# Kernel optimization log

Hardware: AMD Instinct MI355X
Metric: run time of the kernel (lower is better)

Reference implementation:

```python
import jax, jax.numpy as jnp
import numpy as np
import math

N_HEAD = 16
N_KV_HEAD = 4
N_EMBD = 2048
HEAD_DIM = N_EMBD // N_HEAD  # 128
SCALE = 1.0 / math.sqrt(HEAD_DIM)
B, T = 2, 2048


def setup_inputs() -> dict:
    key = jax.random.key(0)
    ks = jax.random.split(key, 5)
    s = 0.02
    x = jax.random.normal(ks[0], (B, T, N_EMBD), dtype=jnp.float32)
    wq = jax.random.normal(ks[1], (N_EMBD, N_EMBD), dtype=jnp.float32) * s
    wk = jax.random.normal(ks[2], (N_KV_HEAD * HEAD_DIM, N_EMBD), dtype=jnp.float32) * s
    wv = jax.random.normal(ks[3], (N_KV_HEAD * HEAD_DIM, N_EMBD), dtype=jnp.float32) * s
    wo = jax.random.normal(ks[4], (N_EMBD, N_EMBD), dtype=jnp.float32) * s
    return {"x": x, "wq": wq, "wk": wk, "wv": wv, "wo": wo}


def _forward(x, wq, wk, wv, wo):
    b, t, _ = x.shape
    # Linear layers: y = x @ W.T  (torch Linear weight is (out,in))
    q = (x @ wq.T).reshape(b, t, N_HEAD, HEAD_DIM).transpose(0, 2, 1, 3)      # (B,H,T,D)
    k = (x @ wk.T).reshape(b, t, N_KV_HEAD, HEAD_DIM).transpose(0, 2, 1, 3)  # (B,Hkv,T,D)
    v = (x @ wv.T).reshape(b, t, N_KV_HEAD, HEAD_DIM).transpose(0, 2, 1, 3)
    groups = N_HEAD // N_KV_HEAD
    k = jnp.repeat(k, groups, axis=1)  # repeat_interleave over head dim -> (B,H,T,D)
    v = jnp.repeat(v, groups, axis=1)
    # Causal mask: True above diagonal (masked-out positions)
    mask = jnp.triu(jnp.ones((t, t), dtype=bool), k=1)[None, None]  # (1,1,T,T)
    scores = jnp.einsum('bhqd,bhkd->bhqk', q, k) * SCALE
    scores = jnp.where(mask, -jnp.inf, scores)
    attn = jax.nn.softmax(scores, axis=-1)
    attn = jnp.where(mask, 0.0, attn)
    y = jnp.einsum('bhqk,bhkd->bhqd', attn, v)       # (B,H,T,D)
    y = y.transpose(0, 2, 1, 3).reshape(b, t, N_EMBD)
    return y @ wo.T


def reference(x, wq, wk, wv, wo):
    return _forward(x, wq, wk, wv, wo)
```

## Files before the change

### kernel.cpp

```cpp
#include <hip/hip_runtime.h>
#include <cstdint>
#include <cstddef>

typedef __bf16 bf16_t;
typedef __bf16 bf16x8 __attribute__((ext_vector_type(8)));
typedef __bf16 bf16x4 __attribute__((ext_vector_type(4)));
typedef float f32x4 __attribute__((ext_vector_type(4)));

#define GL2LDS16(gptr, lptr)                                                   \
  __builtin_amdgcn_global_load_lds(                                            \
      (__attribute__((address_space(1))) void*)(gptr),                         \
      (__attribute__((address_space(3))) void*)(lptr), 16, 0, 0)

__device__ __forceinline__ float fast_exp2(float x) {
  float r;
  asm volatile("v_exp_f32 %0, %1" : "=v"(r) : "v"(x));
  return r;
}

#define BATCH 2
#define T_SEQ 2048
#define NH 16
#define NKV 4
#define HD 128
#define EMB 2048
#define KVDIM (NKV * HD)
#define MROWS (BATCH * T_SEQ)

__global__ void cvt_all(const float4* __restrict__ x,  const float4* __restrict__ wq,
                        const float4* __restrict__ wk, const float4* __restrict__ wv,
                        const float4* __restrict__ wo,
                        bf16x4* __restrict__ xb,  bf16x4* __restrict__ wqb,
                        bf16x4* __restrict__ wkb, bf16x4* __restrict__ wvb,
                        bf16x4* __restrict__ wob) {
  const int blk = blockIdx.x;
  const float4* src;
  bf16x4* dst;
  int base;
  if (blk < 8192)       { src = x;  dst = xb;  base = blk; }
  else if (blk < 12288) { src = wq; dst = wqb; base = blk - 8192; }
  else if (blk < 13312) { src = wk; dst = wkb; base = blk - 12288; }
  else if (blk < 14336) { src = wv; dst = wvb; base = blk - 13312; }
  else                  { src = wo; dst = wob; base = blk - 14336; }
  const int i = base * 256 + threadIdx.x;
  const float4 v = src[i];
  dst[i] = bf16x4{(__bf16)v.x, (__bf16)v.y, (__bf16)v.z, (__bf16)v.w};
}

#define BK8 64
#define NT8 (EMB / BK8)

__global__ __launch_bounds__(512, 2)
void gemm_qkv8(const bf16_t* __restrict__ A,
               const bf16_t* __restrict__ Wq, const bf16_t* __restrict__ Wk,
               const bf16_t* __restrict__ Wv,
               bf16_t* __restrict__ Qb, bf16_t* __restrict__ Kb,
               bf16_t* __restrict__ Vt, float qalpha)
{
  __shared__ bf16_t lds[2][512 * 64];

  const int tid  = threadIdx.x;
  const int lane = tid & 63;
  const int wv   = tid >> 6;
  const int l15  = lane & 15;
  const int lq   = lane >> 4;

  const int bid0 = blockIdx.x;
  const int bid  = (bid0 & 7) * 24 + (bid0 >> 3);
  const int mt = bid / 12, nt = bid % 12;
  const int m0 = mt * 256;

  const bf16_t* Bmat; int ncol0, seg;
  if (nt < 8)       { Bmat = Wq; ncol0 = nt * 256;        seg = 0; }
  else if (nt < 10) { Bmat = Wk; ncol0 = (nt - 8) * 256;  seg = 1; }
  else              { Bmat = Wv; ncol0 = (nt - 10) * 256; seg = 2; }

  const int wm = (wv >> 2) * 128;
  const int wn = (wv & 3) * 64;

  f32x4 acc[8][4] = {};

  auto stage = [&](int dbuf, int tsrc, int h) {
    const int k0 = tsrc * BK8;
    const bf16_t* src = (h < 2) ? A : Bmat;
    const int rbase = (h < 2) ? (m0 + h * 128) : (ncol0 + (h - 2) * 128);
    bf16_t* dst = &lds[dbuf][h * 8192];
#pragma unroll
    for (int r = 0; r < 2; ++r) {
      const int c = r * 512 + tid;
      const int row = c >> 3, p = c & 7;
      const int sb = p ^ (row & 7);
      GL2LDS16(src + (size_t)(rbase + row) * EMB + k0 + sb * 8, dst + c * 8);
    }
  };

  stage(0, 0, 0); stage(0, 0, 1); stage(0, 0, 2); stage(0, 0, 3);
  stage(1, 1, 2); stage(1, 1, 0); stage(1, 1, 3);
  asm volatile("s_waitcnt vmcnt(6)" ::: "memory");
  __builtin_amdgcn_s_barrier();

  bf16x8 a[4][2], b[4][2];

#pragma unroll 1
  for (int tt = 0; tt < NT8; tt += 2) {
#pragma unroll
    for (int u = 0; u < 2; ++u) {
      const int t   = tt + u;
      const int cur = u;
      const int nxt = u ^ 1;
      const int tn1 = (t + 1 < NT8) ? t + 1 : NT8 - 1;
      const int tn2 = (t + 2 < NT8) ? t + 2 : NT8 - 1;

#pragma unroll
      for (int i = 0; i < 4; ++i) {
        const int row = wm + i * 16 + l15;
#pragma unroll
        for (int ks = 0; ks < 2; ++ks)
          a[i][ks] = *(const bf16x8*)&lds[cur][row * 64 + (((ks * 4 + lq) ^ (row & 7)) * 8)];
      }
#pragma unroll
      for (int j = 0; j < 2; ++j) {
        const int row = 256 + wn + j * 16 + l15;
#pragma unroll
        for (int ks = 0; ks < 2; ++ks)
          b[j][ks] = *(const bf16x8*)&lds[cur][row * 64 + (((ks * 4 + lq) ^ (row & 7)) * 8)];
      }
      stage(nxt, tn1, 1);
      __builtin_amdgcn_s_barrier();
      __builtin_amdgcn_s_setprio(1);
#pragma unroll
      for (int ks = 0; ks < 2; ++ks)
#pragma unroll
        for (int i = 0; i < 4; ++i)
#pragma unroll
          for (int j = 0; j < 2; ++j)
            acc[i][j] = __builtin_amdgcn_mfma_f32_16x16x32_bf16(a[i][ks], b[j][ks], acc[i][j], 0, 0, 0);
      __builtin_amdgcn_s_setprio(0);
      __builtin_amdgcn_s_barrier();

#pragma unroll
      for (int j = 2; j < 4; ++j) {
        const int row = 256 + wn + j * 16 + l15;
#pragma unroll
        for (int ks = 0; ks < 2; ++ks)
          b[j][ks] = *(const bf16x8*)&lds[cur][row * 64 + (((ks * 4 + lq) ^ (row & 7)) * 8)];
      }
      __builtin_amdgcn_s_barrier();
      __builtin_amdgcn_s_setprio(1);
#pragma unroll
      for (int ks = 0; ks < 2; ++ks)
#pragma unroll
        for (int i = 0; i < 4; ++i)
#pragma unroll
          for (int j = 2; j < 4; ++j)
            acc[i][j] = __builtin_amdgcn_mfma_f32_16x16x32_bf16(a[i][ks], b[j][ks], acc[i][j], 0, 0, 0);
      __builtin_amdgcn_s_setprio(0);
      __builtin_amdgcn_s_barrier();

#pragma unroll
      for (int i = 0; i < 4; ++i) {
        const int row = wm + (4 + i) * 16 + l15;
#pragma unroll
        for (int ks = 0; ks < 2; ++ks)
          a[i][ks] = *(const bf16x8*)&lds[cur][row * 64 + (((ks * 4 + lq) ^ (row & 7)) * 8)];
      }
      stage(cur, tn2, 2);
      __builtin_amdgcn_s_barrier();
      __builtin_amdgcn_s_setprio(1);
#pragma unroll
      for (int ks = 0; ks < 2; ++ks)
#pragma unroll
        for (int i = 0; i < 4; ++i)
#pragma unroll
          for (int j = 2; j < 4; ++j)
            acc[4 + i][j] = __builtin_amdgcn_mfma_f32_16x16x32_bf16(a[i][ks], b[j][ks], acc[4 + i][j], 0, 0, 0);
      __builtin_amdgcn_s_setprio(0);
      __builtin_amdgcn_s_barrier();

      stage(cur, tn2, 0);
      stage(cur, tn2, 3);
      __builtin_amdgcn_s_barrier();
      __builtin_amdgcn_s_setprio(1);
#pragma unroll
      for (int ks = 0; ks < 2; ++ks)
#pragma unroll
        for (int i = 0; i < 4; ++i)
#pragma unroll
          for (int j = 0; j < 2; ++j)
            acc[4 + i][j] = __builtin_amdgcn_mfma_f32_16x16x32_bf16(a[i][ks], b[j][ks], acc[4 + i][j], 0, 0, 0);
      __builtin_amdgcn_s_setprio(0);
      asm volatile("s_waitcnt vmcnt(6)" ::: "memory");
      __builtin_amdgcn_s_barrier();
    }
  }
  asm volatile("s_waitcnt vmcnt(0)" ::: "memory");

  if (seg == 0) {
#pragma unroll
    for (int i = 0; i < 8; ++i) {
      const int rbase = m0 + wm + i * 16 + lq * 4;
#pragma unroll
      for (int j = 0; j < 4; ++j) {
        const int col = ncol0 + wn + j * 16 + l15;
#pragma unroll
        for (int r = 0; r < 4; ++r)
          Qb[(size_t)(rbase + r) * EMB + col] = (bf16_t)(acc[i][j][r] * qalpha);
      }
    }
  } else if (seg == 1) {
#pragma unroll
    for (int i = 0; i < 8; ++i) {
      const int rbase = m0 + wm + i * 16 + lq * 4;
#pragma unroll
      for (int j = 0; j < 4; ++j) {
        const int col = ncol0 + wn + j * 16 + l15;
#pragma unroll
        for (int r = 0; r < 4; ++r)
          Kb[(size_t)(rbase + r) * KVDIM + col] = (bf16_t)acc[i][j][r];
      }
    }
  } else {
    const int bb = m0 >> 11;
    const int mloc0 = (m0 & 2047) + wm + lq * 4;
#pragma unroll
    for (int i = 0; i < 8; ++i) {
      const int mloc = mloc0 + i * 16;
#pragma unroll
      for (int j = 0; j < 4; ++j) {
        const int d = ncol0 + wn + j * 16 + l15;
        *(bf16x4*)(Vt + (size_t)(bb * KVDIM + d) * T_SEQ + mloc) =
            bf16x4{(__bf16)acc[i][j][0], (__bf16)acc[i][j][1],
                   (__bf16)acc[i][j][2], (__bf16)acc[i][j][3]};
      }
    }
  }
}

__global__ __launch_bounds__(256, 2)
void gemm_out(const bf16_t* __restrict__ A, const bf16_t* __restrict__ Bm,
              float* __restrict__ C, int M, int N, int K)
{
  __shared__ bf16_t As[128 * 64];
  __shared__ bf16_t Bs[128 * 64];

  const int tid  = threadIdx.x;
  const int lane = tid & 63;
  const int wv   = tid >> 6;
  const int m0 = blockIdx.y * 128;
  const int n0 = blockIdx.x * 128;
  const int wm = (wv >> 1) * 64;
  const int wn = (wv & 1) * 64;
  const int l15 = lane & 15;
  const int lq  = lane >> 4;

  f32x4 acc[4][4] = {};
  const int srow = tid >> 3;
  const int scol = (tid & 7) * 8;

  for (int k0 = 0; k0 < K; k0 += 64) {
#pragma unroll
    for (int r = 0; r < 4; ++r) {
      const int row = r * 32 + srow;
      GL2LDS16(A + (size_t)(m0 + row) * K + k0 + scol, As + row * 64 + scol);
    }
#pragma unroll
    for (int r = 0; r < 4; ++r) {
      const int row = r * 32 + srow;
      GL2LDS16(Bm + (size_t)(n0 + row) * K + k0 + scol, Bs + row * 64 + scol);
    }
    __syncthreads();

#pragma unroll
    for (int ks = 0; ks < 2; ++ks) {
      const int kc = ks * 32 + lq * 8;
      bf16x8 af[4], bf[4];
#pragma unroll
      for (int i = 0; i < 4; ++i)
        af[i] = *(const bf16x8*)(As + (wm + i * 16 + l15) * 64 + kc);
#pragma unroll
      for (int j = 0; j < 4; ++j)
        bf[j] = *(const bf16x8*)(Bs + (wn + j * 16 + l15) * 64 + kc);
#pragma unroll
      for (int i = 0; i < 4; ++i)
#pragma unroll
        for (int j = 0; j < 4; ++j)
          acc[i][j] = __builtin_amdgcn_mfma_f32_16x16x32_bf16(af[i], bf[j], acc[i][j], 0, 0, 0);
    }
    __syncthreads();
  }

#pragma unroll
  for (int i = 0; i < 4; ++i) {
    const int rbase = m0 + wm + i * 16 + lq * 4;
#pragma unroll
    for (int j = 0; j < 4; ++j) {
      const int col = n0 + wn + j * 16 + l15;
#pragma unroll
      for (int r = 0; r < 4; ++r)
        C[(size_t)(rbase + r) * N + col] = acc[i][j][r];
    }
  }
}

#define PSTR 72

__global__ __launch_bounds__(256, 2)
void attn_fwd(const bf16_t* __restrict__ Q, const bf16_t* __restrict__ Kg,
              const bf16_t* __restrict__ Vt, bf16_t* __restrict__ Y)
{
  __shared__ bf16_t Ks[2][64 * 128];
  __shared__ bf16_t Vs[2][128 * 64];
  __shared__ bf16_t Ps[4][16 * PSTR];

  const int tid  = threadIdx.x;
  const int lane = tid & 63;
  const int wv   = tid >> 6;
  const int l15  = lane & 15;
  const int lq   = lane >> 4;
  const int h  = blockIdx.y;
  const int b  = blockIdx.z;
  const int hkv = h >> 2;
  bf16_t* Psw = Ps[wv];

  auto stage = [&](int kt, int bufsel) {
    const int base_t = b * T_SEQ + kt * 64;
#pragma unroll
    for (int r = 0; r < 4; ++r) {
      const int c = r * 256 + tid;
      const int row = c >> 4, p = c & 15;
      const int sb = p ^ (row & 7);
      GL2LDS16(Kg + (size_t)(base_t + row) * KVDIM + hkv * HD + sb * 8,
               &Ks[bufsel][c * 8]);
    }
#pragma unroll
    for (int r = 0; r < 4; ++r) {
      const int c = r * 256 + tid;
      const int row = c >> 3, p = c & 7;
      const int sb = p ^ (row & 7);
      GL2LDS16(Vt + (size_t)(b * KVDIM + hkv * HD + row) * T_SEQ + kt * 64 + sb * 8,
               &Vs[bufsel][c * 8]);
    }
  };

#pragma unroll 1
  for (int ph = 0; ph < 2; ++ph) {
    const int qt = ph ? blockIdx.x : (31 - blockIdx.x);
    const int q0 = qt * 64;
    const int nkt = qt + 1;
    const int qabs = q0 + wv * 16 + l15;

    bf16x8 qf[4];
    {
      const bf16_t* qp = Q + ((size_t)(b * T_SEQ + qabs) * NH + h) * HD + lq * 8;
#pragma unroll
      for (int ds = 0; ds < 4; ++ds)
        qf[ds] = *(const bf16x8*)(qp + ds * 32);
    }

    float l_part = 0.f;
    f32x4 o[8];
#pragma unroll
    for (int nb = 0; nb < 8; ++nb) o[nb] = f32x4{0.f, 0.f, 0.f, 0.f};

    __syncthreads();
    stage(0, 0);

    for (int kt = 0; kt < nkt; ++kt) {
      const int cur = kt & 1;
      __syncthreads();
      if (kt + 1 < nkt) stage(kt + 1, cur ^ 1);

      f32x4 s[4];
#pragma unroll
      for (int nb = 0; nb < 4; ++nb) {
        s[nb] = f32x4{0.f, 0.f, 0.f, 0.f};
        const int row = nb * 16 + l15;
        const int r7  = row & 7;
#pragma unroll
        for (int ds = 0; ds < 4; ++ds) {
          const bf16x8 kf = *(const bf16x8*)&Ks[cur][row * 128 + (((ds * 4 + lq) ^ r7) * 8)];
          s[nb] = __builtin_amdgcn_mfma_f32_16x16x32_bf16(kf, qf[ds], s[nb], 0, 0, 0);
        }
      }

      const bool dia = (kt == nkt - 1);
#pragma unroll
      for (int nb = 0; nb < 4; ++nb) {
        const int kvb = kt * 64 + nb * 16 + lq * 4;
        float p0, p1, p2, p3;
        if (dia) {
          p0 = (kvb + 0 <= qabs) ? fast_exp2(s[nb][0]) : 0.f;
          p1 = (kvb + 1 <= qabs) ? fast_exp2(s[nb][1]) : 0.f;
          p2 = (kvb + 2 <= qabs) ? fast_exp2(s[nb][2]) : 0.f;
          p3 = (kvb + 3 <= qabs) ? fast_exp2(s[nb][3]) : 0.f;
        } else {
          p0 = fast_exp2(s[nb][0]);
          p1 = fast_exp2(s[nb][1]);
          p2 = fast_exp2(s[nb][2]);
          p3 = fast_exp2(s[nb][3]);
        }
        l_part += (p0 + p1) + (p2 + p3);
        *(bf16x4*)(Psw + l15 * PSTR + nb * 16 + lq * 4) =
            bf16x4{(__bf16)p0, (__bf16)p1, (__bf16)p2, (__bf16)p3};
      }

      asm volatile("s_waitcnt lgkmcnt(0)" ::: "memory");

#pragma unroll
      for (int ks = 0; ks < 2; ++ks) {
        const bf16x8 pf = *(const bf16x8*)(Psw + l15 * PSTR + ks * 32 + lq * 8);
#pragma unroll
        for (int nb = 0; nb < 8; ++nb) {
          const int row = nb * 16 + l15;
          const bf16x8 vf = *(const bf16x8*)&Vs[cur][row * 64 + (((ks * 4 + lq) ^ (row & 7)) * 8)];
          o[nb] = __builtin_amdgcn_mfma_f32_16x16x32_bf16(vf, pf, o[nb], 0, 0, 0);
        }
      }
    }

    float lt = l_part;
    lt += __shfl_xor(lt, 16);
    lt += __shfl_xor(lt, 32);
    const float inv = 1.f / lt;
    bf16_t* yp = Y + ((size_t)(b * T_SEQ + qabs) * NH + h) * HD + lq * 4;
#pragma unroll
    for (int nb = 0; nb < 8; ++nb) {
      *(bf16x4*)(yp + nb * 16) = bf16x4{(__bf16)(o[nb][0] * inv), (__bf16)(o[nb][1] * inv),
                                        (__bf16)(o[nb][2] * inv), (__bf16)(o[nb][3] * inv)};
    }
  }
}

extern "C" void kernel_launch(void* const* d_in, const int* in_sizes, int n_in,
                              void* d_out, int out_size, void* d_ws, size_t ws_size,
                              hipStream_t stream) {
  const float* x  = (const float*)d_in[0];
  const float* wq = (const float*)d_in[1];
  const float* wk = (const float*)d_in[2];
  const float* wv = (const float*)d_in[3];
  const float* wo = (const float*)d_in[4];
  float* out = (float*)d_out;

  const size_t n_x  = (size_t)MROWS * EMB;
  const size_t n_wq = (size_t)EMB * EMB;
  const size_t n_wk = (size_t)KVDIM * EMB;

  bf16_t* xb  = (bf16_t*)d_ws;
  bf16_t* wqb = xb  + n_x;
  bf16_t* wkb = wqb + n_wq;
  bf16_t* wvb = wkb + n_wk;
  bf16_t* wob = wvb + n_wk;
  bf16_t* Qb  = wob + n_wq;
  bf16_t* Kb  = Qb + (size_t)MROWS * EMB;
  bf16_t* Vtb = Kb + (size_t)MROWS * KVDIM;
  bf16_t* Yb  = Vtb + (size_t)MROWS * KVDIM;

  dim3 blk(256);

  cvt_all<<<dim3(18432), blk, 0, stream>>>(
      (const float4*)x, (const float4*)wq, (const float4*)wk, (const float4*)wv, (const float4*)wo,
      (bf16x4*)xb, (bf16x4*)wqb, (bf16x4*)wkb, (bf16x4*)wvb, (bf16x4*)wob);

  const float qalpha = 0.08838834764831845f * 1.4426950408889634f;
  gemm_qkv8<<<dim3(192), dim3(512), 0, stream>>>(xb, wqb, wkb, wvb,
                                                 Qb, Kb, Vtb, qalpha);

  attn_fwd<<<dim3(16, NH, BATCH), blk, 0, stream>>>(Qb, Kb, Vtb, Yb);

  gemm_out<<<dim3(EMB / 128, MROWS / 128), blk, 0, stream>>>(Yb, wob, out, MROWS, EMB, EMB);
}
```

Before: 278.9 us.

## Software-pipeline LDS fragment loads across MFMA phases in projection GEMM

Restructures the GEMM main loop so LDS fragment reads for the next phase (and the next k-tile's first A/B halves) are issued before the current MFMA block, using separate A/B register sets that alternate between iterations. Barriers per phase drop from two to one, and the global-to-LDS wait is tightened to vmcnt(2) placed before the last stages. This aims to hide LDS read latency behind matrix ops and reduce synchronization stalls. It raises register pressure and relies on subtle wait/barrier ordering for correctness.

After: 316.9 us. 1.14x slower.

```diff
diff --git a/kernel.cpp b/kernel.cpp
--- a/kernel.cpp
+++ b/kernel.cpp
@@ -94,104 +94,77 @@
     }
   };
 
+  auto ldA = [&](int buf, int half, bf16x8 (&dst)[4][2]) {
+#pragma unroll
+    for (int i = 0; i < 4; ++i) {
+      const int row = wm + half * 64 + i * 16 + l15;
+#pragma unroll
+      for (int ks = 0; ks < 2; ++ks)
+        dst[i][ks] = *(const bf16x8*)&lds[buf][row * 64 + (((ks * 4 + lq) ^ (row & 7)) * 8)];
+    }
+  };
+  auto ldB = [&](int buf, int half, bf16x8 (&dst)[2][2]) {
+#pragma unroll
+    for (int j = 0; j < 2; ++j) {
+      const int row = 256 + wn + half * 32 + j * 16 + l15;
+#pragma unroll
+      for (int ks = 0; ks < 2; ++ks)
+        dst[j][ks] = *(const bf16x8*)&lds[buf][row * 64 + (((ks * 4 + lq) ^ (row & 7)) * 8)];
+    }
+  };
+  auto mm = [&](bf16x8 (&Af)[4][2], bf16x8 (&Bf)[2][2], int ai, int bj) {
+    __builtin_amdgcn_s_setprio(1);
+#pragma unroll
+    for (int ks = 0; ks < 2; ++ks)
+#pragma unroll
+      for (int i = 0; i < 4; ++i)
+#pragma unroll
+        for (int j = 0; j < 2; ++j)
+          acc[ai + i][bj + j] = __builtin_amdgcn_mfma_f32_16x16x32_bf16(
+              Af[i][ks], Bf[j][ks], acc[ai + i][bj + j], 0, 0, 0);
+    __builtin_amdgcn_s_setprio(0);
+  };
+
   stage(0, 0, 0); stage(0, 0, 1); stage(0, 0, 2); stage(0, 0, 3);
   stage(1, 1, 2); stage(1, 1, 0); stage(1, 1, 3);
   asm volatile("s_waitcnt vmcnt(6)" ::: "memory");
   __builtin_amdgcn_s_barrier();
 
-  bf16x8 a[4][2], b[4][2];
+  bf16x8 al[4][2], ah[4][2], bX[2][2], bY[2][2];
+  ldA(0, 0, al);
+  ldB(0, 0, bX);
+
+  auto body = [&](int cur, int t, bf16x8 (&b01)[2][2], bf16x8 (&b23)[2][2]) {
+    const int nxt = cur ^ 1;
+    const int tn1 = (t + 1 < NT8) ? t + 1 : NT8 - 1;
+    const int tn2 = (t + 2 < NT8) ? t + 2 : NT8 - 1;
+
+    stage(nxt, tn1, 1);
+    ldB(cur, 1, b23);
+    mm(al, b01, 0, 0);
+    __builtin_amdgcn_s_barrier();
+
+    ldA(cur, 1, ah);
+    mm(al, b23, 0, 2);
+    __builtin_amdgcn_s_barrier();
+
+    stage(cur, tn2, 2);
+    mm(ah, b23, 4, 2);
+    __builtin_amdgcn_s_barrier();
+
+    asm volatile("s_waitcnt vmcnt(2)" ::: "memory");
+    stage(cur, tn2, 0);
+    stage(cur, tn2, 3);
+    ldA(nxt, 0, al);
+    ldB(nxt, 0, b23);
+    mm(ah, b01, 4, 0);
+    __builtin_amdgcn_s_barrier();
+  };
 
 #pragma unroll 1
   for (int tt = 0; tt < NT8; tt += 2) {
-#pragma unroll
-    for (int u = 0; u < 2; ++u) {
-      const int t   = tt + u;
-      const int cur = u;
-      const int nxt = u ^ 1;
-      const int tn1 = (t + 1 < NT8) ? t + 1 : NT8 - 1;
-      const int tn2 = (t + 2 < NT8) ? t + 2 : NT8 - 1;
-
-#pragma unroll
-      for (int i = 0; i < 4; ++i) {
-        const int row = wm + i * 16 + l15;
-#pragma unroll
-        for (int ks = 0; ks < 2; ++ks)
-          a[i][ks] = *(const bf16x8*)&lds[cur][row * 64 + (((ks * 4 + lq) ^ (row & 7)) * 8)];
-      }
-#pragma unroll
-      for (int j = 0; j < 2; ++j) {
-        const int row = 256 + wn + j * 16 + l15;
-#pragma unroll
-        for (int ks = 0; ks < 2; ++ks)
-          b[j][ks] = *(const bf16x8*)&lds[cur][row * 64 + (((ks * 4 + lq) ^ (row & 7)) * 8)];
-      }
-      stage(nxt, tn1, 1);
-      __builtin_amdgcn_s_barrier();
-      __builtin_amdgcn_s_setprio(1);
-#pragma unroll
-      for (int ks = 0; ks < 2; ++ks)
-#pragma unroll
-        for (int i = 0; i < 4; ++i)
-#pragma unroll
-          for (int j = 0; j < 2; ++j)
-            acc[i][j] = __builtin_amdgcn_mfma_f32_16x16x32_bf16(a[i][ks], b[j][ks], acc[i][j], 0, 0, 0);
-      __builtin_amdgcn_s_setprio(0);
-      __builtin_amdgcn_s_barrier();
-
-#pragma unroll
-      for (int j = 2; j < 4; ++j) {
-        const int row = 256 + wn + j * 16 + l15;
-#pragma unroll
-        for (int ks = 0; ks < 2; ++ks)
-          b[j][ks] = *(const bf16x8*)&lds[cur][row * 64 + (((ks * 4 + lq) ^ (row & 7)) * 8)];
-      }
-      __builtin_amdgcn_s_barrier();
-      __builtin_amdgcn_s_setprio(1);
-#pragma unroll
-      for (int ks = 0; ks < 2; ++ks)
-#pragma unroll
-        for (int i = 0; i < 4; ++i)
-#pragma unroll
-          for (int j = 2; j < 4; ++j)
-            acc[i][j] = __builtin_amdgcn_mfma_f32_16x16x32_bf16(a[i][ks], b[j][ks], acc[i][j], 0, 0, 0);
-      __builtin_amdgcn_s_setprio(0);
-      __builtin_amdgcn_s_barrier();
-
-#pragma unroll
-      for (int i = 0; i < 4; ++i) {
-        const int row = wm + (4 + i) * 16 + l15;
-#pragma unroll
-        for (int ks = 0; ks < 2; ++ks)
-          a[i][ks] = *(const bf16x8*)&lds[cur][row * 64 + (((ks * 4 + lq) ^ (row & 7)) * 8)];
-      }
-      stage(cur, tn2, 2);
-      __builtin_amdgcn_s_barrier();
-      __builtin_amdgcn_s_setprio(1);
-#pragma unroll
-      for (int ks = 0; ks < 2; ++ks)
-#pragma unroll
-        for (int i = 0; i < 4; ++i)
-#pragma unroll
-          for (int j = 2; j < 4; ++j)
-            acc[4 + i][j] = __builtin_amdgcn_mfma_f32_16x16x32_bf16(a[i][ks], b[j][ks], acc[4 + i][j], 0, 0, 0);
-      __builtin_amdgcn_s_setprio(0);
-      __builtin_amdgcn_s_barrier();
-
-      stage(cur, tn2, 0);
-      stage(cur, tn2, 3);
-      __builtin_amdgcn_s_barrier();
-      __builtin_amdgcn_s_setprio(1);
-#pragma unroll
-      for (int ks = 0; ks < 2; ++ks)
-#pragma unroll
-        for (int i = 0; i < 4; ++i)
-#pragma unroll
-          for (int j = 0; j < 2; ++j)
-            acc[4 + i][j] = __builtin_amdgcn_mfma_f32_16x16x32_bf16(a[i][ks], b[j][ks], acc[4 + i][j], 0, 0, 0);
-      __builtin_amdgcn_s_setprio(0);
-      asm volatile("s_waitcnt vmcnt(6)" ::: "memory");
-      __builtin_amdgcn_s_barrier();
-    }
+    body(0, tt,     bX, bY);
+    body(1, tt + 1, bY, bX);
   }
   asm volatile("s_waitcnt vmcnt(0)" ::: "memory");
 
```

## Double attention query tile per block to reuse K/V tiles across 32 rows per wave

Applied to the files above, without the earlier changes.

Each wave of the attention kernel now handles 32 query rows (two 16-row MFMA tiles) instead of 16, so each block covers 128 queries. Every K/V tile staged into LDS feeds twice as many MFMAs, which halves global K/V traffic and per-tile sync overhead. The grid shrinks to 256 blocks and launch bounds drop to one block per CU to allow the extra accumulator registers. The cost is fewer resident waves for latency hiding, fewer blocks to balance the causal work across CUs, and a larger LDS P buffer.

Result: slower. 301.9 us (+8.3%).

```diff
diff --git a/kernel.cpp b/kernel.cpp
--- a/kernel.cpp
+++ b/kernel.cpp
@@ -304,13 +304,13 @@
 
 #define PSTR 72
 
-__global__ __launch_bounds__(256, 2)
+__global__ __launch_bounds__(256, 1)
 void attn_fwd(const bf16_t* __restrict__ Q, const bf16_t* __restrict__ Kg,
               const bf16_t* __restrict__ Vt, bf16_t* __restrict__ Y)
 {
   __shared__ bf16_t Ks[2][64 * 128];
   __shared__ bf16_t Vs[2][128 * 64];
-  __shared__ bf16_t Ps[4][16 * PSTR];
+  __shared__ bf16_t Ps[4][32 * PSTR];
 
   const int tid  = threadIdx.x;
   const int lane = tid & 63;
@@ -344,23 +344,30 @@
 
 #pragma unroll 1
   for (int ph = 0; ph < 2; ++ph) {
-    const int qt = ph ? blockIdx.x : (31 - blockIdx.x);
-    const int q0 = qt * 64;
-    const int nkt = qt + 1;
-    const int qabs = q0 + wv * 16 + l15;
-
-    bf16x8 qf[4];
+    const int qt = ph ? blockIdx.x : (15 - blockIdx.x);
+    const int q0 = qt * 128;
+    const int nkt = 2 * qt + 2;
+    const int qa0 = q0 + wv * 32 + l15;
+    const int qa1 = qa0 + 16;
+
+    bf16x8 qf0[4], qf1[4];
     {
-      const bf16_t* qp = Q + ((size_t)(b * T_SEQ + qabs) * NH + h) * HD + lq * 8;
-#pragma unroll
-      for (int ds = 0; ds < 4; ++ds)
-        qf[ds] = *(const bf16x8*)(qp + ds * 32);
-    }
-
-    float l_part = 0.f;
-    f32x4 o[8];
-#pragma unroll
-    for (int nb = 0; nb < 8; ++nb) o[nb] = f32x4{0.f, 0.f, 0.f, 0.f};
+      const bf16_t* qp0 = Q + ((size_t)(b * T_SEQ + qa0) * NH + h) * HD + lq * 8;
+      const bf16_t* qp1 = Q + ((size_t)(b * T_SEQ + qa1) * NH + h) * HD + lq * 8;
+#pragma unroll
+      for (int ds = 0; ds < 4; ++ds) {
+        qf0[ds] = *(const bf16x8*)(qp0 + ds * 32);
+        qf1[ds] = *(const bf16x8*)(qp1 + ds * 32);
+      }
+    }
+
+    float l0 = 0.f, l1 = 0.f;
+    f32x4 o0[8], o1[8];
+#pragma unroll
+    for (int nb = 0; nb < 8; ++nb) {
+      o0[nb] = f32x4{0.f, 0.f, 0.f, 0.f};
+      o1[nb] = f32x4{0.f, 0.f, 0.f, 0.f};
+    }
 
     __syncthreads();
     stage(0, 0);
@@ -370,63 +377,88 @@
       __syncthreads();
       if (kt + 1 < nkt) stage(kt + 1, cur ^ 1);
 
-      f32x4 s[4];
+      f32x4 s0[4], s1[4];
 #pragma unroll
       for (int nb = 0; nb < 4; ++nb) {
-        s[nb] = f32x4{0.f, 0.f, 0.f, 0.f};
+        s0[nb] = f32x4{0.f, 0.f, 0.f, 0.f};
+        s1[nb] = f32x4{0.f, 0.f, 0.f, 0.f};
         const int row = nb * 16 + l15;
         const int r7  = row & 7;
 #pragma unroll
         for (int ds = 0; ds < 4; ++ds) {
           const bf16x8 kf = *(const bf16x8*)&Ks[cur][row * 128 + (((ds * 4 + lq) ^ r7) * 8)];
-          s[nb] = __builtin_amdgcn_mfma_f32_16x16x32_bf16(kf, qf[ds], s[nb], 0, 0, 0);
+          s0[nb] = __builtin_amdgcn_mfma_f32_16x16x32_bf16(kf, qf0[ds], s0[nb], 0, 0, 0);
+          s1[nb] = __builtin_amdgcn_mfma_f32_16x16x32_bf16(kf, qf1[ds], s1[nb], 0, 0, 0);
         }
       }
 
-      const bool dia = (kt == nkt - 1);
+      const bool dia = (kt >= nkt - 2);
 #pragma unroll
       for (int nb = 0; nb < 4; ++nb) {
         const int kvb = kt * 64 + nb * 16 + lq * 4;
         float p0, p1, p2, p3;
         if (dia) {
-          p0 = (kvb + 0 <= qabs) ? fast_exp2(s[nb][0]) : 0.f;
-          p1 = (kvb + 1 <= qabs) ? fast_exp2(s[nb][1]) : 0.f;
-          p2 = (kvb + 2 <= qabs) ? fast_exp2(s[nb][2]) : 0.f;
-          p3 = (kvb + 3 <= qabs) ? fast_exp2(s[nb][3]) : 0.f;
+          p0 = (kvb + 0 <= qa0) ? fast_exp2(s0[nb][0]) : 0.f;
+          p1 = (kvb + 1 <= qa0) ? fast_exp2(s0[nb][1]) : 0.f;
+          p2 = (kvb + 2 <= qa0) ? fast_exp2(s0[nb][2]) : 0.f;
+          p3 = (kvb + 3 <= qa0) ? fast_exp2(s0[nb][3]) : 0.f;
         } else {
-          p0 = fast_exp2(s[nb][0]);
-          p1 = fast_exp2(s[nb][1]);
-          p2 = fast_exp2(s[nb][2]);
-          p3 = fast_exp2(s[nb][3]);
+          p0 = fast_exp2(s0[nb][0]);
+          p1 = fast_exp2(s0[nb][1]);
+          p2 = fast_exp2(s0[nb][2]);
+          p3 = fast_exp2(s0[nb][3]);
         }
-        l_part += (p0 + p1) + (p2 + p3);
+        l0 += (p0 + p1) + (p2 + p3);
         *(bf16x4*)(Psw + l15 * PSTR + nb * 16 + lq * 4) =
             bf16x4{(__bf16)p0, (__bf16)p1, (__bf16)p2, (__bf16)p3};
+
+        if (dia) {
+          p0 = (kvb + 0 <= qa1) ? fast_exp2(s1[nb][0]) : 0.f;
+          p1 = (kvb + 1 <= qa1) ? fast_exp2(s1[nb][1]) : 0.f;
+          p2 = (kvb + 2 <= qa1) ? fast_exp2(s1[nb][2]) : 0.f;
+          p3 = (kvb + 3 <= qa1) ? fast_exp2(s1[nb][3]) : 0.f;
+        } else {
+          p0 = fast_exp2(s1[nb][0]);
+          p1 = fast_exp2(s1[nb][1]);
+          p2 = fast_exp2(s1[nb][2]);
+          p3 = fast_exp2(s1[nb][3]);
+        }
+        l1 += (p0 + p1) + (p2 + p3);
+        *(bf16x4*)(Psw + (16 + l15) * PSTR + nb * 16 + lq * 4) =
+            bf16x4{(__bf16)p0, (__bf16)p1, (__bf16)p2, (__bf16)p3};
       }
 
       asm volatile("s_waitcnt lgkmcnt(0)" ::: "memory");
 
 #pragma unroll
       for (int ks = 0; ks < 2; ++ks) {
-        const bf16x8 pf = *(const bf16x8*)(Psw + l15 * PSTR + ks * 32 + lq * 8);
+        const bf16x8 pf0 = *(const bf16x8*)(Psw + l15 * PSTR + ks * 32 + lq * 8);
+        const bf16x8 pf1 = *(const bf16x8*)(Psw + (16 + l15) * PSTR + ks * 32 + lq * 8);
 #pragma unroll
         for (int nb = 0; nb < 8; ++nb) {
           const int row = nb * 16 + l15;
           const bf16x8 vf = *(const bf16x8*)&Vs[cur][row * 64 + (((ks * 4 + lq) ^ (row & 7)) * 8)];
-          o[nb] = __builtin_amdgcn_mfma_f32_16x16x32_bf16(vf, pf, o[nb], 0, 0, 0);
+          o0[nb] = __builtin_amdgcn_mfma_f32_16x16x32_bf16(vf, pf0, o0[nb], 0, 0, 0);
+          o1[nb] = __builtin_amdgcn_mfma_f32_16x16x32_bf16(vf, pf1, o1[nb], 0, 0, 0);
         }
       }
     }
 
-    float lt = l_part;
-    lt += __shfl_xor(lt, 16);
-    lt += __shfl_xor(lt, 32);
-    const float inv = 1.f / lt;
-    bf16_t* yp = Y + ((size_t)(b * T_SEQ + qabs) * NH + h) * HD + lq * 4;
+    float lt0 = l0, lt1 = l1;
+    lt0 += __shfl_xor(lt0, 16);
+    lt0 += __shfl_xor(lt0, 32);
+    lt1 += __shfl_xor(lt1, 16);
+    lt1 += __shfl_xor(lt1, 32);
+    const float inv0 = 1.f / lt0;
+    const float inv1 = 1.f / lt1;
+    bf16_t* yp0 = Y + ((size_t)(b * T_SEQ + qa0) * NH + h) * HD + lq * 4;
+    bf16_t* yp1 = Y + ((size_t)(b * T_SEQ + qa1) * NH + h) * HD + lq * 4;
 #pragma unroll
     for (int nb = 0; nb < 8; ++nb) {
-      *(bf16x4*)(yp + nb * 16) = bf16x4{(__bf16)(o[nb][0] * inv), (__bf16)(o[nb][1] * inv),
-                                        (__bf16)(o[nb][2] * inv), (__bf16)(o[nb][3] * inv)};
+      *(bf16x4*)(yp0 + nb * 16) = bf16x4{(__bf16)(o0[nb][0] * inv0), (__bf16)(o0[nb][1] * inv0),
+                                         (__bf16)(o0[nb][2] * inv0), (__bf16)(o0[nb][3] * inv0)};
+      *(bf16x4*)(yp1 + nb * 16) = bf16x4{(__bf16)(o1[nb][0] * inv1), (__bf16)(o1[nb][1] * inv1),
+                                         (__bf16)(o1[nb][2] * inv1), (__bf16)(o1[nb][3] * inv1)};
     }
   }
 }
@@ -465,7 +497,7 @@
   gemm_qkv8<<<dim3(192), dim3(512), 0, stream>>>(xb, wqb, wkb, wvb,
                                                  Qb, Kb, Vtb, qalpha);
 
-  attn_fwd<<<dim3(16, NH, BATCH), blk, 0, stream>>>(Qb, Kb, Vtb, Yb);
+  attn_fwd<<<dim3(8, NH, BATCH), blk, 0, stream>>>(Qb, Kb, Vtb, Yb);
 
   gemm_out<<<dim3(EMB / 128, MROWS / 128), blk, 0, stream>>>(Yb, wob, out, MROWS, EMB, EMB);
 }
```

## Split attention KV range across two wave groups and merge partial outputs

Applied to the files above, without the earlier changes.

The attention kernel now uses 512-thread blocks, one per query tile, instead of 256-thread blocks that each handled a pair of causally balanced tiles. Two groups of four waves each take half of the KV range with 32-row KV tiles. Their partial outputs and row sums are combined through shared memory at the end. This raises parallelism and occupancy, at the cost of a reduction step, smaller tiles with more barriers per unit of work, and imbalance across blocks from the causal tile sizes.

Result: slower. 333.6 us (+19.6%).

```diff
diff --git a/kernel.cpp b/kernel.cpp
--- a/kernel.cpp
+++ b/kernel.cpp
@@ -302,19 +302,21 @@
   }
 }
 
-#define PSTR 72
-
-__global__ __launch_bounds__(256, 2)
+#define PSTR 40
+
+__global__ __launch_bounds__(512, 4)
 void attn_fwd(const bf16_t* __restrict__ Q, const bf16_t* __restrict__ Kg,
               const bf16_t* __restrict__ Vt, bf16_t* __restrict__ Y)
 {
-  __shared__ bf16_t Ks[2][64 * 128];
-  __shared__ bf16_t Vs[2][128 * 64];
-  __shared__ bf16_t Ps[4][16 * PSTR];
+  __shared__ bf16_t Ksm[2][2][32 * 128];
+  __shared__ bf16_t Vsm[2][2][128 * 32];
+  __shared__ bf16_t Ps[8][16 * PSTR];
 
   const int tid  = threadIdx.x;
   const int lane = tid & 63;
   const int wv   = tid >> 6;
+  const int grp  = wv >> 2;
+  const int gtid = tid & 255;
   const int l15  = lane & 15;
   const int lq   = lane >> 4;
   const int h  = blockIdx.y;
@@ -322,111 +324,122 @@
   const int hkv = h >> 2;
   bf16_t* Psw = Ps[wv];
 
-  auto stage = [&](int kt, int bufsel) {
-    const int base_t = b * T_SEQ + kt * 64;
-#pragma unroll
-    for (int r = 0; r < 4; ++r) {
-      const int c = r * 256 + tid;
+  const int qt  = 31 - blockIdx.x;
+  const int q0  = qt * 64;
+  const int niter = qt + 1;
+  const int qabs = q0 + (wv & 3) * 16 + l15;
+
+  auto stage = [&](int kt, int buf) {
+    const int base_t = b * T_SEQ + kt * 32;
+#pragma unroll
+    for (int r = 0; r < 2; ++r) {
+      const int c = r * 256 + gtid;
       const int row = c >> 4, p = c & 15;
       const int sb = p ^ (row & 7);
       GL2LDS16(Kg + (size_t)(base_t + row) * KVDIM + hkv * HD + sb * 8,
-               &Ks[bufsel][c * 8]);
-    }
-#pragma unroll
-    for (int r = 0; r < 4; ++r) {
-      const int c = r * 256 + tid;
-      const int row = c >> 3, p = c & 7;
-      const int sb = p ^ (row & 7);
-      GL2LDS16(Vt + (size_t)(b * KVDIM + hkv * HD + row) * T_SEQ + kt * 64 + sb * 8,
-               &Vs[bufsel][c * 8]);
+               &Ksm[grp][buf][c * 8]);
+    }
+#pragma unroll
+    for (int r = 0; r < 2; ++r) {
+      const int c = r * 256 + gtid;
+      const int row = c >> 2, p = c & 3;
+      const int sb = p ^ (row & 3);
+      GL2LDS16(Vt + (size_t)(b * KVDIM + hkv * HD + row) * T_SEQ + kt * 32 + sb * 8,
+               &Vsm[grp][buf][c * 8]);
     }
   };
 
-#pragma unroll 1
-  for (int ph = 0; ph < 2; ++ph) {
-    const int qt = ph ? blockIdx.x : (31 - blockIdx.x);
-    const int q0 = qt * 64;
-    const int nkt = qt + 1;
-    const int qabs = q0 + wv * 16 + l15;
-
-    bf16x8 qf[4];
+  bf16x8 qf[4];
+  {
+    const bf16_t* qp = Q + ((size_t)(b * T_SEQ + qabs) * NH + h) * HD + lq * 8;
+#pragma unroll
+    for (int ds = 0; ds < 4; ++ds)
+      qf[ds] = *(const bf16x8*)(qp + ds * 32);
+  }
+
+  float l_part = 0.f;
+  f32x4 o[8];
+#pragma unroll
+  for (int nb = 0; nb < 8; ++nb) o[nb] = f32x4{0.f, 0.f, 0.f, 0.f};
+
+  const int kt0 = grp ? niter : 0;
+  stage(kt0, 0);
+
+  for (int i = 0; i < niter; ++i) {
+    const int cur = i & 1;
+    __syncthreads();
+    if (i + 1 < niter) stage(kt0 + i + 1, cur ^ 1);
+    const int kt = kt0 + i;
+    const bool dia = (kt * 32 + 31 >= q0);
+
+    f32x4 s[2];
+#pragma unroll
+    for (int nb = 0; nb < 2; ++nb) {
+      s[nb] = f32x4{0.f, 0.f, 0.f, 0.f};
+      const int row = nb * 16 + l15;
+      const int r7  = row & 7;
+#pragma unroll
+      for (int ds = 0; ds < 4; ++ds) {
+        const bf16x8 kf = *(const bf16x8*)&Ksm[grp][cur][row * 128 + (((ds * 4 + lq) ^ r7) * 8)];
+        s[nb] = __builtin_amdgcn_mfma_f32_16x16x32_bf16(kf, qf[ds], s[nb], 0, 0, 0);
+      }
+    }
+
+#pragma unroll
+    for (int nb = 0; nb < 2; ++nb) {
+      const int kvb = kt * 32 + nb * 16 + lq * 4;
+      float p0, p1, p2, p3;
+      if (dia) {
+        p0 = (kvb + 0 <= qabs) ? fast_exp2(s[nb][0]) : 0.f;
+        p1 = (kvb + 1 <= qabs) ? fast_exp2(s[nb][1]) : 0.f;
+        p2 = (kvb + 2 <= qabs) ? fast_exp2(s[nb][2]) : 0.f;
+        p3 = (kvb + 3 <= qabs) ? fast_exp2(s[nb][3]) : 0.f;
+      } else {
+        p0 = fast_exp2(s[nb][0]); p1 = fast_exp2(s[nb][1]);
+        p2 = fast_exp2(s[nb][2]); p3 = fast_exp2(s[nb][3]);
+      }
+      l_part += (p0 + p1) + (p2 + p3);
+      *(bf16x4*)(Psw + l15 * PSTR + nb * 16 + lq * 4) =
+          bf16x4{(__bf16)p0, (__bf16)p1, (__bf16)p2, (__bf16)p3};
+    }
+
+    asm volatile("s_waitcnt lgkmcnt(0)" ::: "memory");
+
     {
-      const bf16_t* qp = Q + ((size_t)(b * T_SEQ + qabs) * NH + h) * HD + lq * 8;
-#pragma unroll
-      for (int ds = 0; ds < 4; ++ds)
-        qf[ds] = *(const bf16x8*)(qp + ds * 32);
-    }
-
-    float l_part = 0.f;
-    f32x4 o[8];
-#pragma unroll
-    for (int nb = 0; nb < 8; ++nb) o[nb] = f32x4{0.f, 0.f, 0.f, 0.f};
-
-    __syncthreads();
-    stage(0, 0);
-
-    for (int kt = 0; kt < nkt; ++kt) {
-      const int cur = kt & 1;
-      __syncthreads();
-      if (kt + 1 < nkt) stage(kt + 1, cur ^ 1);
-
-      f32x4 s[4];
-#pragma unroll
-      for (int nb = 0; nb < 4; ++nb) {
-        s[nb] = f32x4{0.f, 0.f, 0.f, 0.f};
+      const bf16x8 pf = *(const bf16x8*)(Psw + l15 * PSTR + lq * 8);
+#pragma unroll
+      for (int nb = 0; nb < 8; ++nb) {
         const int row = nb * 16 + l15;
-        const int r7  = row & 7;
-#pragma unroll
-        for (int ds = 0; ds < 4; ++ds) {
-          const bf16x8 kf = *(const bf16x8*)&Ks[cur][row * 128 + (((ds * 4 + lq) ^ r7) * 8)];
-          s[nb] = __builtin_amdgcn_mfma_f32_16x16x32_bf16(kf, qf[ds], s[nb], 0, 0, 0);
-        }
-      }
-
-      const bool dia = (kt == nkt - 1);
-#pragma unroll
-      for (int nb = 0; nb < 4; ++nb) {
-        const int kvb = kt * 64 + nb * 16 + lq * 4;
-        float p0, p1, p2, p3;
-        if (dia) {
-          p0 = (kvb + 0 <= qabs) ? fast_exp2(s[nb][0]) : 0.f;
-          p1 = (kvb + 1 <= qabs) ? fast_exp2(s[nb][1]) : 0.f;
-          p2 = (kvb + 2 <= qabs) ? fast_exp2(s[nb][2]) : 0.f;
-          p3 = (kvb + 3 <= qabs) ? fast_exp2(s[nb][3]) : 0.f;
-        } else {
-          p0 = fast_exp2(s[nb][0]);
-          p1 = fast_exp2(s[nb][1]);
-          p2 = fast_exp2(s[nb][2]);
-          p3 = fast_exp2(s[nb][3]);
-        }
-        l_part += (p0 + p1) + (p2 + p3);
-        *(bf16x4*)(Psw + l15 * PSTR + nb * 16 + lq * 4) =
-            bf16x4{(__bf16)p0, (__bf16)p1, (__bf16)p2, (__bf16)p3};
-      }
-
-      asm volatile("s_waitcnt lgkmcnt(0)" ::: "memory");
-
-#pragma unroll
-      for (int ks = 0; ks < 2; ++ks) {
-        const bf16x8 pf = *(const bf16x8*)(Psw + l15 * PSTR + ks * 32 + lq * 8);
-#pragma unroll
-        for (int nb = 0; nb < 8; ++nb) {
-          const int row = nb * 16 + l15;
-          const bf16x8 vf = *(const bf16x8*)&Vs[cur][row * 64 + (((ks * 4 + lq) ^ (row & 7)) * 8)];
-          o[nb] = __builtin_amdgcn_mfma_f32_16x16x32_bf16(vf, pf, o[nb], 0, 0, 0);
-        }
-      }
-    }
-
-    float lt = l_part;
-    lt += __shfl_xor(lt, 16);
-    lt += __shfl_xor(lt, 32);
-    const float inv = 1.f / lt;
+        const bf16x8 vf = *(const bf16x8*)&Vsm[grp][cur][row * 32 + ((lq ^ (row & 3)) * 8)];
+        o[nb] = __builtin_amdgcn_mfma_f32_16x16x32_bf16(vf, pf, o[nb], 0, 0, 0);
+      }
+    }
+  }
+
+  __syncthreads();
+  if (grp == 1) {
+    const int w = wv & 3;
+    float* dst = (w < 2 ? (float*)&Ksm[1][0][0] : (float*)&Vsm[1][0][0]) +
+                 (w & 1) * 2048 + lane * 32;
+#pragma unroll
+    for (int nb = 0; nb < 8; ++nb) *(f32x4*)(dst + nb * 4) = o[nb];
+    ((float*)Ps[4 + w])[lane] = l_part;
+  }
+  __syncthreads();
+  if (grp == 0) {
+    const int w = wv;
+    const float* src = (w < 2 ? (const float*)&Ksm[1][0][0] : (const float*)&Vsm[1][0][0]) +
+                       (w & 1) * 2048 + lane * 32;
+    float lp = l_part + ((const float*)Ps[4 + w])[lane];
+    lp += __shfl_xor(lp, 16);
+    lp += __shfl_xor(lp, 32);
+    const float inv = 1.f / lp;
     bf16_t* yp = Y + ((size_t)(b * T_SEQ + qabs) * NH + h) * HD + lq * 4;
 #pragma unroll
     for (int nb = 0; nb < 8; ++nb) {
-      *(bf16x4*)(yp + nb * 16) = bf16x4{(__bf16)(o[nb][0] * inv), (__bf16)(o[nb][1] * inv),
-                                        (__bf16)(o[nb][2] * inv), (__bf16)(o[nb][3] * inv)};
+      const f32x4 ob = o[nb] + *(const f32x4*)(src + nb * 4);
+      *(bf16x4*)(yp + nb * 16) = bf16x4{(__bf16)(ob[0] * inv), (__bf16)(ob[1] * inv),
+                                        (__bf16)(ob[2] * inv), (__bf16)(ob[3] * inv)};
     }
   }
 }
@@ -465,7 +478,7 @@
   gemm_qkv8<<<dim3(192), dim3(512), 0, stream>>>(xb, wqb, wkb, wvb,
                                                  Qb, Kb, Vtb, qalpha);
 
-  attn_fwd<<<dim3(16, NH, BATCH), blk, 0, stream>>>(Qb, Kb, Vtb, Yb);
+  attn_fwd<<<dim3(32, NH, BATCH), dim3(512), 0, stream>>>(Qb, Kb, Vtb, Yb);
 
   gemm_out<<<dim3(EMB / 128, MROWS / 128), blk, 0, stream>>>(Yb, wob, out, MROWS, EMB, EMB);
 }
```
